# Optimization experiments

Measured on AMD Instinct MI355X. Metric: run time of the kernel, lower is better.

## Reference

```python
import jax, jax.numpy as jnp
import numpy as np

KH, KW = 3, 3          # kernel_size
STRIDE, PAD, DIL = 1, 1, 1
DG = 1                 # deformable_groups


def setup_inputs() -> dict:
    key = jax.random.key(0)
    k1, k2 = jax.random.split(key)
    x = jax.random.normal(k1, (4, 64, 128, 128), dtype=jnp.float32)
    # offset layout: [B, 2*DG*KH*KW, Ho, Wo], pairs are (dy, dx) per tap
    offset = jax.random.normal(k2, (4, 2 * DG * KH * KW, 128, 128), dtype=jnp.float32)
    return {"input": x, "offset": offset}


def _deform_unfold(x, offset):
    B, C, H, W = x.shape
    Ho = (H + 2 * PAD - DIL * (KH - 1) - 1) // STRIDE + 1
    Wo = (W + 2 * PAD - DIL * (KW - 1) - 1) // STRIDE + 1
    K = KH * KW
    Cg = C // DG

    off = offset.reshape(B, DG, K, 2, Ho, Wo)
    oy, ox = off[:, :, :, 0], off[:, :, :, 1]          # [B,DG,K,Ho,Wo]

    # tap displacements within the kernel window
    ky = (jnp.repeat(jnp.arange(KH), KW) * DIL).astype(x.dtype)  # [K]
    kx = (jnp.tile(jnp.arange(KW), KH) * DIL).astype(x.dtype)    # [K]
    gy = (jnp.arange(Ho) * STRIDE - PAD).astype(x.dtype)         # [Ho]
    gx = (jnp.arange(Wo) * STRIDE - PAD).astype(x.dtype)         # [Wo]

    # fractional sampling coordinates  [B,DG,K,Ho,Wo]
    py = oy + gy[None, None, None, :, None] + ky[None, None, :, None, None]
    px = ox + gx[None, None, None, None, :] + kx[None, None, :, None, None]

    y0 = jnp.floor(py)
    x0 = jnp.floor(px)
    wy1 = py - y0
    wx1 = px - x0
    wy0 = 1.0 - wy1
    wx0 = 1.0 - wx1
    y0i = y0.astype(jnp.int32)
    x0i = x0.astype(jnp.int32)

    x_flat = x.reshape(B, DG, Cg, H * W)

    def corner(yi, xi, w):
        valid = ((yi >= 0) & (yi < H) & (xi >= 0) & (xi < W)).astype(x.dtype)
        idx = jnp.clip(yi, 0, H - 1) * W + jnp.clip(xi, 0, W - 1)   # [B,DG,K,Ho,Wo]
        idxf = idx.reshape(B, DG, K * Ho * Wo)
        # gather: xf [Cg,HW], ix [N] -> [Cg,N]; vmapped over B and DG
        g = jax.vmap(jax.vmap(lambda xf, ix: xf[:, ix]))(x_flat, idxf)
        g = g.reshape(B, DG, Cg, K, Ho, Wo)
        return g * (w * valid)[:, :, None]        # broadcast over Cg

    out = (corner(y0i, x0i, wy0 * wx0)
           + corner(y0i, x0i + 1, wy0 * wx1)
           + corner(y0i + 1, x0i, wy1 * wx0)
           + corner(y0i + 1, x0i + 1, wy1 * wx1))   # [B,DG,Cg,K,Ho,Wo]

    # im2col layout: channel-major, tap-minor -> [B, C*K, Ho*Wo]
    return out.reshape(B, C * K, Ho * Wo)


def reference(input, offset):
    return _deform_unfold(input, offset)
```

## Files before the change

### kernel.cpp

```cpp
#include <hip/hip_runtime.h>


#define BB 4
#define CC 64
#define HH 128
#define WW 128
#define KK 9
#define HW (HH * WW)
#define NR 16
#define CG 8
#define NG (CC / CG)
#define TPB 256

__global__ __launch_bounds__(TPB, 4) void deform_unfold_lds(
    const float* __restrict__ x, const float* __restrict__ off,
    float* __restrict__ out)
{
    __shared__ float2 tile[NR * WW];
    __shared__ int anyfall;

    const int tid = threadIdx.x;
    const int bid = blockIdx.x;
    const int g = bid & (NG - 1);
    const int t = (bid >> 3) & 63;
    const int b = bid >> 9;

    const int s  = t * TPB + tid;
    const int wo = s & (WW - 1);
    const int ho = s >> 7;
    const int r0 = min(max(2 * t - 6, 0), HH - NR);

    const int c0g = g * CG;
    const float* xb = x + ((size_t)b * CC + c0g) * HW;
    float* ob = out + (((size_t)b * CC + c0g) * KK) * HW + s;

    float2 pa[4], pb[4];
    {
        const float2* A2 = (const float2*)(xb + (size_t)r0 * WW);
        const float2* B2 = (const float2*)(xb + HW + (size_t)r0 * WW);
        #pragma unroll
        for (int j = 0; j < 4; ++j) { pa[j] = A2[tid + 256 * j]; pb[j] = B2[tid + 256 * j]; }
    }

    if (tid == 0) anyfall = 0;
    __syncthreads();

    float u0[KK], u1[KK], t0w[KK], t1w[KK];
    int aAB[KK];
    int myfall = 0;
    #pragma unroll
    for (int k = 0; k < KK; ++k) {
        int ky = k / 3, kx = k - ky * 3;
        float oy = off[(((size_t)b * (2 * KK)) + 2 * k) * HW + s];
        float ox = off[(((size_t)b * (2 * KK)) + 2 * k + 1) * HW + s];
        float py = oy + (float)(ho - 1 + ky);
        float px = ox + (float)(wo - 1 + kx);
        float y0f = floorf(py), x0f = floorf(px);
        float wy1 = py - y0f, wx1 = px - x0f;
        float wy0 = 1.f - wy1, wx0 = 1.f - wx1;
        int y0 = (int)y0f, x0 = (int)x0f;
        int y1 = y0 + 1, x1 = x0 + 1;
        bool vy0 = (y0 >= 0) && (y0 < HH), vy1 = (y1 >= 0) && (y1 < HH);
        bool vx0 = (x0 >= 0) && (x0 < WW), vx1 = (x1 >= 0) && (x1 < WW);
        int y0c = min(max(y0, 0), HH - 1), y1c = min(max(y1, 0), HH - 1);
        int xa  = min(max(x0, 0), WW - 2);
        int i0  = min(max(x0, 0), WW - 1) - xa;
        int i1  = min(max(x1, 0), WW - 1) - xa;
        float w00 = wy0 * wx0 * ((vy0 && vx0) ? 1.f : 0.f);
        float w01 = wy0 * wx1 * ((vy0 && vx1) ? 1.f : 0.f);
        float w10 = wy1 * wx0 * ((vy1 && vx0) ? 1.f : 0.f);
        float w11 = wy1 * wx1 * ((vy1 && vx1) ? 1.f : 0.f);
        u0[k]  = (i0 == 0 ? w00 : 0.f) + (i1 == 0 ? w01 : 0.f);
        u1[k]  = (i0 == 1 ? w00 : 0.f) + (i1 == 1 ? w01 : 0.f);
        t0w[k] = (i0 == 0 ? w10 : 0.f) + (i1 == 0 ? w11 : 0.f);
        t1w[k] = (i0 == 1 ? w10 : 0.f) + (i1 == 1 ? w11 : 0.f);
        int rA = y0c - r0, rB = y1c - r0;
        myfall |= ((unsigned)rA >= NR) | ((unsigned)rB >= NR);
        rA = min(max(rA, 0), NR - 1);
        rB = min(max(rB, 0), NR - 1);
        aAB[k] = (rA * WW + xa) | ((rB * WW + xa) << 16);
    }
    if (myfall) atomicOr(&anyfall, 1);
    __syncthreads();
    const bool fall = (anyfall != 0);

    if (!fall) {
        #pragma unroll
        for (int cp = 0; cp < CG / 2; ++cp) {
            float4* wt = (float4*)tile;
            #pragma unroll
            for (int j = 0; j < 4; ++j)
                wt[tid + 256 * j] = make_float4(pa[j].x, pb[j].x, pa[j].y, pb[j].y);
            if (cp + 1 < CG / 2) {
                const float2* A2 = (const float2*)(xb + (size_t)(2 * cp + 2) * HW + (size_t)r0 * WW);
                const float2* B2 = (const float2*)(xb + (size_t)(2 * cp + 3) * HW + (size_t)r0 * WW);
                #pragma unroll
                for (int j = 0; j < 4; ++j) { pa[j] = A2[tid + 256 * j]; pb[j] = B2[tid + 256 * j]; }
            }
            __syncthreads();
            float* o = ob + (size_t)(2 * cp) * KK * HW;
            #pragma unroll
            for (int k = 0; k < KK; ++k) {
                int aA = aAB[k] & 0xffff, aB = aAB[k] >> 16;
                float2 p00 = tile[aA], p01 = tile[aA + 1];
                float2 p10 = tile[aB], p11 = tile[aB + 1];
                float vx_ = p00.x * u0[k] + p01.x * u1[k] + p10.x * t0w[k] + p11.x * t1w[k];
                float vy_ = p00.y * u0[k] + p01.y * u1[k] + p10.y * t0w[k] + p11.y * t1w[k];
                __builtin_nontemporal_store(vx_, o + (size_t)k * HW);
                __builtin_nontemporal_store(vy_, o + (size_t)(KK + k) * HW);
            }
            __syncthreads();
        }
    } else {
        #pragma unroll 1
        for (int k = 0; k < KK; ++k) {
            int ky = k / 3, kx = k - ky * 3;
            float oy = off[(((size_t)b * (2 * KK)) + 2 * k) * HW + s];
            float ox = off[(((size_t)b * (2 * KK)) + 2 * k + 1) * HW + s];
            float py = oy + (float)(ho - 1 + ky);
            float px = ox + (float)(wo - 1 + kx);
            float y0f = floorf(py), x0f = floorf(px);
            float wy1 = py - y0f, wx1 = px - x0f;
            float wy0 = 1.f - wy1, wx0 = 1.f - wx1;
            int y0 = (int)y0f, x0 = (int)x0f;
            int y1 = y0 + 1, x1 = x0 + 1;
            bool vy0 = (y0 >= 0) && (y0 < HH), vy1 = (y1 >= 0) && (y1 < HH);
            bool vx0 = (x0 >= 0) && (x0 < WW), vx1 = (x1 >= 0) && (x1 < WW);
            int y0c = min(max(y0, 0), HH - 1), y1c = min(max(y1, 0), HH - 1);
            int x0c = min(max(x0, 0), WW - 1), x1c = min(max(x1, 0), WW - 1);
            float w00 = wy0 * wx0 * ((vy0 && vx0) ? 1.f : 0.f);
            float w01 = wy0 * wx1 * ((vy0 && vx1) ? 1.f : 0.f);
            float w10 = wy1 * wx0 * ((vy1 && vx0) ? 1.f : 0.f);
            float w11 = wy1 * wx1 * ((vy1 && vx1) ? 1.f : 0.f);
            int o00 = y0c * WW + x0c, o01 = y0c * WW + x1c;
            int o10 = y1c * WW + x0c, o11 = y1c * WW + x1c;
            #pragma unroll 1
            for (int c = 0; c < CG; ++c) {
                const float* xc = xb + (size_t)c * HW;
                (ob + (size_t)c * KK * HW)[(size_t)k * HW] =
                    xc[o00] * w00 + xc[o01] * w01 + xc[o10] * w10 + xc[o11] * w11;
            }
        }
    }
}

extern "C" void kernel_launch(void* const* d_in, const int* in_sizes, int n_in,
                              void* d_out, int out_size, void* d_ws, size_t ws_size,
                              hipStream_t stream) {
    const float* x   = (const float*)d_in[0];
    const float* off = (const float*)d_in[1];
    float* out = (float*)d_out;

    int blocks = BB * 64 * NG;
    deform_unfold_lds<<<blocks, TPB, 0, stream>>>(x, off, out);
}
```

Before: 37.97 us.

## Double-buffer LDS tile and use lgkmcnt-only barrier to overlap prefetch

Splits the shared tile into two buffers so each channel pair writes a fresh buffer, removing the second block barrier per iteration. The barrier is replaced with an explicit s_waitcnt lgkmcnt(0) plus s_barrier so that in-flight global prefetch loads are not forced to complete at the barrier. This doubles LDS use per block and drops the min-blocks launch bound, which may change occupancy or register allocation.

```diff
diff --git a/kernel.cpp b/kernel.cpp
--- a/kernel.cpp
+++ b/kernel.cpp
@@ -12,11 +12,18 @@
 #define NG (CC / CG)
 #define TPB 256
 
-__global__ __launch_bounds__(TPB, 4) void deform_unfold_lds(
+#define LDS_BARRIER()                                         \
+    do {                                                      \
+        asm volatile("s_waitcnt lgkmcnt(0)" ::: "memory");    \
+        __builtin_amdgcn_s_barrier();                         \
+        asm volatile("" ::: "memory");                        \
+    } while (0)
+
+__global__ __launch_bounds__(TPB) void deform_unfold_lds(
     const float* __restrict__ x, const float* __restrict__ off,
     float* __restrict__ out)
 {
-    __shared__ float2 tile[NR * WW];
+    __shared__ float2 tile[2][NR * WW];
     __shared__ int anyfall;
 
     const int tid = threadIdx.x;
@@ -34,12 +41,12 @@
     const float* xb = x + ((size_t)b * CC + c0g) * HW;
     float* ob = out + (((size_t)b * CC + c0g) * KK) * HW + s;
 
-    float2 pa[4], pb[4];
+    float2 ca[4], cb[4];
     {
         const float2* A2 = (const float2*)(xb + (size_t)r0 * WW);
         const float2* B2 = (const float2*)(xb + HW + (size_t)r0 * WW);
         #pragma unroll
-        for (int j = 0; j < 4; ++j) { pa[j] = A2[tid + 256 * j]; pb[j] = B2[tid + 256 * j]; }
+        for (int j = 0; j < 4; ++j) { ca[j] = A2[tid + 256 * j]; cb[j] = B2[tid + 256 * j]; }
     }
 
     if (tid == 0) anyfall = 0;
@@ -85,31 +92,36 @@
     const bool fall = (anyfall != 0);
 
     if (!fall) {
+        int cur = 0;
         #pragma unroll
         for (int cp = 0; cp < CG / 2; ++cp) {
-            float4* wt = (float4*)tile;
-            #pragma unroll
-            for (int j = 0; j < 4; ++j)
-                wt[tid + 256 * j] = make_float4(pa[j].x, pb[j].x, pa[j].y, pb[j].y);
+            float2 na[4], nb[4];
             if (cp + 1 < CG / 2) {
                 const float2* A2 = (const float2*)(xb + (size_t)(2 * cp + 2) * HW + (size_t)r0 * WW);
                 const float2* B2 = (const float2*)(xb + (size_t)(2 * cp + 3) * HW + (size_t)r0 * WW);
                 #pragma unroll
-                for (int j = 0; j < 4; ++j) { pa[j] = A2[tid + 256 * j]; pb[j] = B2[tid + 256 * j]; }
+                for (int j = 0; j < 4; ++j) { na[j] = A2[tid + 256 * j]; nb[j] = B2[tid + 256 * j]; }
             }
-            __syncthreads();
+            float4* wt = (float4*)tile[cur];
+            #pragma unroll
+            for (int j = 0; j < 4; ++j)
+                wt[tid + 256 * j] = make_float4(ca[j].x, cb[j].x, ca[j].y, cb[j].y);
+            LDS_BARRIER();
+            const float2* tl = tile[cur];
             float* o = ob + (size_t)(2 * cp) * KK * HW;
             #pragma unroll
             for (int k = 0; k < KK; ++k) {
                 int aA = aAB[k] & 0xffff, aB = aAB[k] >> 16;
-                float2 p00 = tile[aA], p01 = tile[aA + 1];
-                float2 p10 = tile[aB], p11 = tile[aB + 1];
+                float2 p00 = tl[aA], p01 = tl[aA + 1];
+                float2 p10 = tl[aB], p11 = tl[aB + 1];
                 float vx_ = p00.x * u0[k] + p01.x * u1[k] + p10.x * t0w[k] + p11.x * t1w[k];
                 float vy_ = p00.y * u0[k] + p01.y * u1[k] + p10.y * t0w[k] + p11.y * t1w[k];
                 __builtin_nontemporal_store(vx_, o + (size_t)k * HW);
                 __builtin_nontemporal_store(vy_, o + (size_t)(KK + k) * HW);
             }
-            __syncthreads();
+            #pragma unroll
+            for (int j = 0; j < 4; ++j) { ca[j] = na[j]; cb[j] = nb[j]; }
+            cur ^= 1;
         }
     } else {
         #pragma unroll 1
```

Measured after the change: 38.93 us. 1.03x slower.
